# Kernel optimization log

Hardware: AMD Instinct MI355X
Metric: run time of the kernel (lower is better)

Reference implementation:

```python
import jax, jax.numpy as jnp
import numpy as np

N_EMBED = 288
HEAD_SIZE = 32


def setup_inputs() -> dict:
    key = jax.random.key(0)
    kx, kk, kq, kv = jax.random.split(key, 4)
    B, T, C = 16, 2048, N_EMBED
    scale = 1.0 / np.sqrt(C)
    return {
        "x": jax.random.normal(kx, (B, T, C), dtype=jnp.float32),
        # Linear(n_embed, head_size, bias=False) weights, stored as [C, head_size]
        "Wk": jax.random.normal(kk, (C, HEAD_SIZE), dtype=jnp.float32) * scale,
        "Wq": jax.random.normal(kq, (C, HEAD_SIZE), dtype=jnp.float32) * scale,
        "Wv": jax.random.normal(kv, (C, HEAD_SIZE), dtype=jnp.float32) * scale,
    }


def reference(x, Wk, Wq, Wv):
    # x: [B, T, C]
    k = x @ Wk  # [B, T, hs]
    q = x @ Wq
    v = x @ Wv
    # NOTE: source computes k @ q^T (not q @ k^T) -- reproduce faithfully.
    weights = jnp.einsum("bth,bsh->bts", k, q) * (HEAD_SIZE ** -0.5)  # [B, T, T]
    T = x.shape[1]
    causal = jnp.tril(jnp.ones((T, T), dtype=bool))
    weights = jnp.where(causal, weights, -jnp.inf)
    weights = jax.nn.softmax(weights, axis=-1)
    return weights @ v  # [B, T, hs]
```

## Files before the change

kernel.cpp:

```cpp
#include <hip/hip_runtime.h>

typedef __bf16 bf16;
typedef __attribute__((ext_vector_type(8))) __bf16 bf16x8;
typedef __attribute__((ext_vector_type(4))) float f32x4;

#define BATCH 16
#define SEQ   2048
#define CEMB  288
#define HS    32
#define NROWS (BATCH * SEQ)

#define XSTR 296

__global__ __launch_bounds__(384, 3) void proj_kernel(
    const float* __restrict__ x, const float* __restrict__ Wk,
    const float* __restrict__ Wq, const float* __restrict__ Wv,
    bf16* __restrict__ Kx, bf16* __restrict__ Qm, bf16* __restrict__ VT)
{
    __shared__ __align__(16) bf16 Xl[32 * XSTR];

    const int tid  = threadIdx.x;
    const int wv   = tid >> 6;
    const int lane = tid & 63;
    const int quad = lane >> 4;
    const int ln   = lane & 15;
    const int dsel = wv >> 1;
    const int half = wv & 1;

    const float SCALE = 0.25519486439582695f;

    const float* Wsrc = (dsel == 0) ? Wk : ((dsel == 1) ? Wq : Wv);
    const float mul = (dsel == 0) ? SCALE : 1.0f;
    bf16x8 wfrag[9];
    for (int kc = 0; kc < 9; ++kc) {
        bf16x8 f;
#pragma unroll
        for (int j = 0; j < 8; ++j) {
            float w = Wsrc[(kc * 32 + quad * 8 + j) * HS + half * 16 + ln];
            f[j] = (bf16)(w * mul);
        }
        wfrag[kc] = f;
    }

    const int wgRowBase = blockIdx.x * 64;
    for (int it = 0; it < 2; ++it) {
        __syncthreads();
        const int rb = wgRowBase + it * 32;
#pragma unroll
        for (int i = 0; i < 6; ++i) {
            int f = tid + 384 * i;
            int row = f / 72;
            int c4  = f - row * 72;
            f32x4 v = ((const f32x4*)x)[(rb + row) * 72 + c4];
            bf16* d = &Xl[row * XSTR + c4 * 4];
            d[0] = (bf16)v[0]; d[1] = (bf16)v[1];
            d[2] = (bf16)v[2]; d[3] = (bf16)v[3];
        }
        __syncthreads();

#pragma unroll
        for (int m = 0; m < 2; ++m) {
            f32x4 acc = {0.f, 0.f, 0.f, 0.f};
#pragma unroll
            for (int kc = 0; kc < 9; ++kc) {
                bf16x8 a = *(const bf16x8*)&Xl[(m * 16 + ln) * XSTR + kc * 32 + quad * 8];
                acc = __builtin_amdgcn_mfma_f32_16x16x32_bf16(a, wfrag[kc], acc, 0, 0, 0);
            }
#pragma unroll
            for (int reg = 0; reg < 4; ++reg) {
                int gr = rb + m * 16 + quad * 4 + reg;
                bf16 val = (bf16)acc[reg];
                if (dsel == 0) {
                    Kx[gr * HS + half * 16 + ln] = val;
                } else if (dsel == 1) {
                    Qm[gr * HS + half * 16 + ln] = val;
                } else {
                    VT[(gr >> 11) * (HS * SEQ) + (half * 16 + ln) * SEQ + (gr & 2047)] = val;
                }
            }
        }
    }
}

#define PSTR 72

__constant__ unsigned char MAP_TILE[72] = {
    15,15,15,15,15,15,15,
    14,14,14,14,14,14,14,
    13,13,13,13,13,13,
    12,12,12,12,12,12,
    11,11,11,11,11,
    10,10,10,10,10,
    9,9,9,9,
    8,8,8,8,
    7,7,7,
    6,6,6,
    5,5,
    4,4,
    3,
    2,
    15,13,11,9,7,5,3,1,
    14,12,10,8,6,4,2,0 };
__constant__ unsigned char MAP_CHUNK[72] = {
    0,1,2,3,4,5,6,
    0,1,2,3,4,5,6,
    0,1,2,3,4,5,
    0,1,2,3,4,5,
    0,1,2,3,4,
    0,1,2,3,4,
    0,1,2,3,
    0,1,2,3,
    0,1,2,
    0,1,2,
    0,1,
    0,1,
    0,
    0,
    7,6,5,4,3,2,1,0,
    7,6,5,4,3,2,1,0 };

__global__ __launch_bounds__(256, 4) void attn_kernel(
    const bf16* __restrict__ Kx, const bf16* __restrict__ Qm,
    const bf16* __restrict__ VT,
    float* __restrict__ Opart, float* __restrict__ Lpart)
{
    __shared__ __align__(16) bf16 Pl[4][2][16 * PSTR];

    const int tid  = threadIdx.x;
    const int w    = tid >> 6;
    const int lane = tid & 63;
    const int quad = lane >> 4;
    const int ln   = lane & 15;

    const int bid   = blockIdx.x;
    const int u     = bid >> 4;
    const int b     = ((bid & 7) << 1) | ((bid >> 3) & 1);
    const int tile  = MAP_TILE[u];
    const int chunk = MAP_CHUNK[u];
    const int t0    = tile * 128;
    const int cs    = chunk * 256;
    const int ce    = min(cs + 256, t0 + 128);

    const bf16* Kb = Kx + b * SEQ * HS;
    const bf16* Qb = Qm + b * SEQ * HS;
    const bf16* Vb = VT + b * HS * SEQ;

    int tsub[2];
    bf16x8 kfrag[2];
#pragma unroll
    for (int m = 0; m < 2; ++m) {
        tsub[m] = t0 + w * 32 + m * 16;
        kfrag[m] = *(const bf16x8*)&Kb[(tsub[m] + ln) * HS + quad * 8];
    }
    bf16x8 ones;
#pragma unroll
    for (int j = 0; j < 8; ++j) ones[j] = (bf16)1.0f;

    f32x4 Of[2][2] = {};
    f32x4 Lf[2]    = {};

    for (int s0 = cs; s0 < ce; s0 += 64) {
        if (s0 >= tsub[1] + 16) break;

        bf16x8 qf[4];
#pragma unroll
        for (int ss = 0; ss < 4; ++ss)
            qf[ss] = *(const bf16x8*)&Qb[(s0 + ss * 16 + ln) * HS + quad * 8];
        bf16x8 vf[2][2];
#pragma unroll
        for (int hb = 0; hb < 2; ++hb)
#pragma unroll
            for (int kb = 0; kb < 2; ++kb)
                vf[hb][kb] = *(const bf16x8*)&Vb[(hb * 16 + ln) * SEQ + s0 + kb * 32 + quad * 8];

#pragma unroll
        for (int m = 0; m < 2; ++m) {
            if (s0 >= tsub[m] + 16) continue;
            const bool diagstep = (s0 + 63 > tsub[m]);
            bf16* P = &Pl[w][m][0];

#pragma unroll
            for (int ss = 0; ss < 4; ++ss) {
                if (s0 + ss * 16 > tsub[m] + 15) {
#pragma unroll
                    for (int reg = 0; reg < 4; ++reg)
                        P[(quad * 4 + reg) * PSTR + ss * 16 + ln] = (bf16)0.0f;
                    continue;
                }
                f32x4 z = {0.f, 0.f, 0.f, 0.f};
                f32x4 S = __builtin_amdgcn_mfma_f32_16x16x32_bf16(kfrag[m], qf[ss], z, 0, 0, 0);
#pragma unroll
                for (int reg = 0; reg < 4; ++reg) {
                    float p = __builtin_amdgcn_exp2f(S[reg]);
                    if (diagstep) {
                        int s = s0 + ss * 16 + ln;
                        int t = tsub[m] + quad * 4 + reg;
                        p = (s <= t) ? p : 0.0f;
                    }
                    P[(quad * 4 + reg) * PSTR + ss * 16 + ln] = (bf16)p;
                }
            }

            bf16x8 ap0 = *(const bf16x8*)&P[ln * PSTR + quad * 8];
            Of[m][0] = __builtin_amdgcn_mfma_f32_16x16x32_bf16(ap0, vf[0][0], Of[m][0], 0, 0, 0);
            Of[m][1] = __builtin_amdgcn_mfma_f32_16x16x32_bf16(ap0, vf[1][0], Of[m][1], 0, 0, 0);
            Lf[m]    = __builtin_amdgcn_mfma_f32_16x16x32_bf16(ap0, ones,    Lf[m],    0, 0, 0);
            if (s0 + 32 <= tsub[m] + 15) {
                bf16x8 ap1 = *(const bf16x8*)&P[ln * PSTR + 32 + quad * 8];
                Of[m][0] = __builtin_amdgcn_mfma_f32_16x16x32_bf16(ap1, vf[0][1], Of[m][0], 0, 0, 0);
                Of[m][1] = __builtin_amdgcn_mfma_f32_16x16x32_bf16(ap1, vf[1][1], Of[m][1], 0, 0, 0);
                Lf[m]    = __builtin_amdgcn_mfma_f32_16x16x32_bf16(ap1, ones,    Lf[m],    0, 0, 0);
            }
        }
    }

#pragma unroll
    for (int m = 0; m < 2; ++m) {
        if (cs >= tsub[m] + 16) continue;
#pragma unroll
        for (int reg = 0; reg < 4; ++reg) {
            int gr = b * SEQ + tsub[m] + quad * 4 + reg;
            float* od = Opart + ((size_t)chunk * NROWS + gr) * HS;
            od[ln]      = Of[m][0][reg];
            od[16 + ln] = Of[m][1][reg];
            if (ln == 0) Lpart[chunk * NROWS + gr] = Lf[m][reg];
        }
    }
}

__global__ __launch_bounds__(256) void combine_kernel(
    const float* __restrict__ Opart, const float* __restrict__ Lpart,
    float* __restrict__ out)
{
    int idx = blockIdx.x * 256 + threadIdx.x;
    int gr = idx >> 3, h4 = idx & 7;
    int t  = gr & 2047;
    int nc = (t >> 8) + 1;
    f32x4 acc = {0.f, 0.f, 0.f, 0.f};
    float l = 0.f;
    for (int c = 0; c < nc; ++c) {
        acc += ((const f32x4*)Opart)[((size_t)c * NROWS + gr) * 8 + h4];
        l   += Lpart[c * NROWS + gr];
    }
    f32x4 r = acc / l;
    ((f32x4*)out)[idx] = r;
}

extern "C" void kernel_launch(void* const* d_in, const int* in_sizes, int n_in,
                              void* d_out, int out_size, void* d_ws, size_t ws_size,
                              hipStream_t stream) {
    (void)in_sizes; (void)n_in; (void)out_size; (void)ws_size;
    const float* x  = (const float*)d_in[0];
    const float* Wk = (const float*)d_in[1];
    const float* Wq = (const float*)d_in[2];
    const float* Wv = (const float*)d_in[3];

    char* ws = (char*)d_ws;
    bf16*  Kx    = (bf16*)(ws);
    bf16*  Qm    = (bf16*)(ws + 2097152);
    bf16*  VT    = (bf16*)(ws + 4194304);
    float* Opart = (float*)(ws + 6291456);
    float* Lpart = (float*)(ws + 6291456 + 33554432);
    float* out   = (float*)d_out;

    hipLaunchKernelGGL(proj_kernel, dim3(512), dim3(384), 0, stream,
                       x, Wk, Wq, Wv, Kx, Qm, VT);
    hipLaunchKernelGGL(attn_kernel, dim3(1152), dim3(256), 0, stream,
                       Kx, Qm, VT, Opart, Lpart);
    hipLaunchKernelGGL(combine_kernel, dim3(1024), dim3(256), 0, stream,
                       Opart, Lpart, out);
}
```

Measured before the change: 109.8 us.

## Keep attention probabilities in registers by transposing S MFMA and permuting Q rows

Swaps the S MFMA operands (Q as A, K as B) and permutes the Q row loads so each lane's output registers line up with the A-operand layout of the PV MFMA. The probabilities can then be packed straight into a bf16x8 fragment with no LDS round trip, and the shared P buffer is removed. The row-sum is now accumulated in fp32 registers and reduced with cross-lane shuffles instead of an extra MFMA against a ones vector. The price is an extra S MFMA per 32-column chunk and more scalar adds, in exchange for dropping the LDS stores and loads.

```diff
diff --git a/kernel.cpp b/kernel.cpp
--- a/kernel.cpp
+++ b/kernel.cpp
@@ -82,7 +82,6 @@
     }
 }
 
-#define PSTR 72
 
 __constant__ unsigned char MAP_TILE[72] = {
     15,15,15,15,15,15,15,
@@ -124,8 +123,6 @@
     const bf16* __restrict__ VT,
     float* __restrict__ Opart, float* __restrict__ Lpart)
 {
-    __shared__ __align__(16) bf16 Pl[4][2][16 * PSTR];
-
     const int tid  = threadIdx.x;
     const int w    = tid >> 6;
     const int lane = tid & 63;
@@ -152,64 +149,64 @@
         tsub[m] = t0 + w * 32 + m * 16;
         kfrag[m] = *(const bf16x8*)&Kb[(tsub[m] + ln) * HS + quad * 8];
     }
-    bf16x8 ones;
-#pragma unroll
-    for (int j = 0; j < 8; ++j) ones[j] = (bf16)1.0f;
+
+    const int qrow = 8 * (ln >> 2) + (ln & 3);
+    const int t_row = ln;
 
     f32x4 Of[2][2] = {};
-    f32x4 Lf[2]    = {};
+    float Lacc[2]  = {0.f, 0.f};
 
     for (int s0 = cs; s0 < ce; s0 += 64) {
         if (s0 >= tsub[1] + 16) break;
 
-        bf16x8 qf[4];
-#pragma unroll
-        for (int ss = 0; ss < 4; ++ss)
-            qf[ss] = *(const bf16x8*)&Qb[(s0 + ss * 16 + ln) * HS + quad * 8];
+        bf16x8 qfA[2], qfB[2];
+#pragma unroll
+        for (int c = 0; c < 2; ++c) {
+            qfA[c] = *(const bf16x8*)&Qb[(s0 + 32 * c + qrow) * HS + quad * 8];
+            qfB[c] = *(const bf16x8*)&Qb[(s0 + 32 * c + qrow + 4) * HS + quad * 8];
+        }
         bf16x8 vf[2][2];
 #pragma unroll
         for (int hb = 0; hb < 2; ++hb)
 #pragma unroll
-            for (int kb = 0; kb < 2; ++kb)
-                vf[hb][kb] = *(const bf16x8*)&Vb[(hb * 16 + ln) * SEQ + s0 + kb * 32 + quad * 8];
+            for (int c = 0; c < 2; ++c)
+                vf[hb][c] = *(const bf16x8*)&Vb[(hb * 16 + ln) * SEQ + s0 + c * 32 + quad * 8];
 
 #pragma unroll
         for (int m = 0; m < 2; ++m) {
-            if (s0 >= tsub[m] + 16) continue;
-            const bool diagstep = (s0 + 63 > tsub[m]);
-            bf16* P = &Pl[w][m][0];
-
-#pragma unroll
-            for (int ss = 0; ss < 4; ++ss) {
-                if (s0 + ss * 16 > tsub[m] + 15) {
-#pragma unroll
-                    for (int reg = 0; reg < 4; ++reg)
-                        P[(quad * 4 + reg) * PSTR + ss * 16 + ln] = (bf16)0.0f;
-                    continue;
+            const int t = tsub[m] + t_row;
+#pragma unroll
+            for (int c = 0; c < 2; ++c) {
+                const int sb = s0 + 32 * c;
+                if (sb >= tsub[m] + 16) continue;
+                const bool diag = (sb + 31 > tsub[m]);
+
+                f32x4 z = {0.f, 0.f, 0.f, 0.f};
+                f32x4 SA = __builtin_amdgcn_mfma_f32_16x16x32_bf16(qfA[c], kfrag[m], z, 0, 0, 0);
+                f32x4 SB = __builtin_amdgcn_mfma_f32_16x16x32_bf16(qfB[c], kfrag[m], z, 0, 0, 0);
+
+                const int sAb = sb + 8 * quad;
+                float pA[4], pB[4];
+#pragma unroll
+                for (int r = 0; r < 4; ++r) {
+                    pA[r] = __builtin_amdgcn_exp2f(SA[r]);
+                    pB[r] = __builtin_amdgcn_exp2f(SB[r]);
+                    if (diag) {
+                        pA[r] = (sAb + r     <= t) ? pA[r] : 0.0f;
+                        pB[r] = (sAb + r + 4 <= t) ? pB[r] : 0.0f;
+                    }
+                    Lacc[m] += pA[r] + pB[r];
                 }
-                f32x4 z = {0.f, 0.f, 0.f, 0.f};
-                f32x4 S = __builtin_amdgcn_mfma_f32_16x16x32_bf16(kfrag[m], qf[ss], z, 0, 0, 0);
-#pragma unroll
-                for (int reg = 0; reg < 4; ++reg) {
-                    float p = __builtin_amdgcn_exp2f(S[reg]);
-                    if (diagstep) {
-                        int s = s0 + ss * 16 + ln;
-                        int t = tsub[m] + quad * 4 + reg;
-                        p = (s <= t) ? p : 0.0f;
-                    }
-                    P[(quad * 4 + reg) * PSTR + ss * 16 + ln] = (bf16)p;
+
+                bf16x8 ap;
+#pragma unroll
+                for (int r = 0; r < 4; ++r) {
+                    ap[r]     = (bf16)pA[r];
+                    ap[r + 4] = (bf16)pB[r];
                 }
-            }
-
-            bf16x8 ap0 = *(const bf16x8*)&P[ln * PSTR + quad * 8];
-            Of[m][0] = __builtin_amdgcn_mfma_f32_16x16x32_bf16(ap0, vf[0][0], Of[m][0], 0, 0, 0);
-            Of[m][1] = __builtin_amdgcn_mfma_f32_16x16x32_bf16(ap0, vf[1][0], Of[m][1], 0, 0, 0);
-            Lf[m]    = __builtin_amdgcn_mfma_f32_16x16x32_bf16(ap0, ones,    Lf[m],    0, 0, 0);
-            if (s0 + 32 <= tsub[m] + 15) {
-                bf16x8 ap1 = *(const bf16x8*)&P[ln * PSTR + 32 + quad * 8];
-                Of[m][0] = __builtin_amdgcn_mfma_f32_16x16x32_bf16(ap1, vf[0][1], Of[m][0], 0, 0, 0);
-                Of[m][1] = __builtin_amdgcn_mfma_f32_16x16x32_bf16(ap1, vf[1][1], Of[m][1], 0, 0, 0);
-                Lf[m]    = __builtin_amdgcn_mfma_f32_16x16x32_bf16(ap1, ones,    Lf[m],    0, 0, 0);
+
+                Of[m][0] = __builtin_amdgcn_mfma_f32_16x16x32_bf16(ap, vf[0][c], Of[m][0], 0, 0, 0);
+                Of[m][1] = __builtin_amdgcn_mfma_f32_16x16x32_bf16(ap, vf[1][c], Of[m][1], 0, 0, 0);
             }
         }
     }
@@ -223,8 +220,12 @@
             float* od = Opart + ((size_t)chunk * NROWS + gr) * HS;
             od[ln]      = Of[m][0][reg];
             od[16 + ln] = Of[m][1][reg];
-            if (ln == 0) Lpart[chunk * NROWS + gr] = Lf[m][reg];
-        }
+        }
+        float l = Lacc[m];
+        l += __shfl_xor(l, 16, 64);
+        l += __shfl_xor(l, 32, 64);
+        if (quad == 0)
+            Lpart[chunk * NROWS + b * SEQ + tsub[m] + ln] = l;
     }
 }
 
```

New measurement: 107.7 us. About the same (-1.9%).
